# Performance work log

Measured on AMD Instinct MI355X. Metric: run time of the kernel, lower is better.

Reference implementation:

```python
import jax, jax.numpy as jnp
import numpy as np
import math

B, C, H, W = 8, 96, 128, 128


def cos_map(N):
    wx = (jnp.arange(N, dtype=jnp.float32) + 0.5) / N          # [N]
    wn = jnp.arange(N, dtype=jnp.float32)[:, None]             # [N,1]
    w = jnp.cos(wn * wx[None, :] * jnp.pi) * math.sqrt(2.0 / N)
    return w.at[0, :].multiply(1.0 / math.sqrt(2.0))            # [N,N] (n, x)


def decay_map(h, w):
    wn = jnp.linspace(0.0, jnp.pi, h + 1)[:h][:, None]
    wm = jnp.linspace(0.0, jnp.pi, w + 1)[:w][None, :]
    return jnp.exp(-(wn ** 2 + wm ** 2))                        # [h,w]


def setup_inputs() -> dict:
    key = jax.random.key(0)
    ks = jax.random.split(key, 20)
    s = 0.02
    return {
        'x': jax.random.normal(ks[0], (B, C, H, W), jnp.float32),
        'freq_embed': jax.random.normal(ks[1], (H, W, C), jnp.float32),
        'outline_feat': jax.random.normal(ks[2], (B, H, W, C), jnp.float32),
        'dw_w': jax.random.normal(ks[3], (C, 1, 3, 3), jnp.float32) * s,
        'dw_b': jnp.zeros((C,), jnp.float32),
        'lin_w': jax.random.normal(ks[4], (2 * C, C), jnp.float32) * s,
        'lin_b': jnp.zeros((2 * C,), jnp.float32),
        'k_w': jax.random.normal(ks[5], (C, C), jnp.float32) * s,
        'k_b': jnp.zeros((C,), jnp.float32),
        'lin2_w': jax.random.normal(ks[6], (2 * C, 2 * C), jnp.float32) * s,
        'lin2_b': jnp.zeros((2 * C,), jnp.float32),
        'k2_w': jax.random.normal(ks[7], (2 * C, 2 * C), jnp.float32) * s,
        'k2_b': jnp.zeros((2 * C,), jnp.float32),
        'lin3_w': jax.random.normal(ks[8], (C, 2 * C), jnp.float32) * s,
        'lin3_b': jnp.zeros((C,), jnp.float32),
        'ln_g': jnp.ones((C,), jnp.float32),
        'ln_b': jnp.zeros((C,), jnp.float32),
        'out_w': jax.random.normal(ks[9], (C, C), jnp.float32) * s,
        'out_b': jnp.zeros((C,), jnp.float32),
    }


def dct2(u, cn, cm):
    # u: [B,H,W,C] -> [B,N,M,C]
    u = jnp.einsum('nh,bhwc->bnwc', cn, u)
    return jnp.einsum('mw,bnwc->bnmc', cm, u)


def idct2(u, cn, cm):
    # u: [B,N,M,C] -> [B,H,W,C]
    u = jnp.einsum('nh,bnmc->bhmc', cn, u)
    return jnp.einsum('mw,bhmc->bhwc', cm, u)


def layernorm(u, g, b, eps=1e-5):
    mu = jnp.mean(u, axis=-1, keepdims=True)
    var = jnp.var(u, axis=-1, keepdims=True)
    return (u - mu) * jax.lax.rsqrt(var + eps) * g + b


def reference(x, freq_embed, outline_feat, dw_w, dw_b, lin_w, lin_b, k_w, k_b,
              lin2_w, lin2_b, k2_w, k2_b, lin3_w, lin3_b, ln_g, ln_b, out_w, out_b):
    # depthwise 3x3 conv, padding 1 (NCHW)
    x = jax.lax.conv_general_dilated(
        x, dw_w, window_strides=(1, 1), padding=((1, 1), (1, 1)),
        dimension_numbers=('NCHW', 'OIHW', 'NCHW'), feature_group_count=C)
    x = x + dw_b[None, :, None, None]
    x = jnp.transpose(x, (0, 2, 3, 1))                          # [B,H,W,C]
    h = jnp.einsum('bhwc,dc->bhwd', x, lin_w) + lin_b           # [B,H,W,2C]
    x, z = jnp.split(h, 2, axis=-1)

    cn, cm = cos_map(H), cos_map(W)
    dec = decay_map(H, W)                                       # [H,W]

    # first heat pass
    x = dct2(x, cn, cm)                                         # [B,N,M,C]
    otfeat = jnp.mean(outline_feat, axis=0)                     # [H,W,C]
    k = jax.nn.relu(jnp.einsum('hwc,dc->hwd', freq_embed + otfeat, k_w) + k_b)
    x = x * jnp.power(dec[:, :, None], k)                       # [B,N,M,C]
    x = idct2(x, cn, cm)                                        # [B,H,W,C]

    # second heat pass on concatenated features
    x = jnp.concatenate([x, outline_feat], axis=-1)             # [B,H,W,2C]
    skfeat = jnp.mean(jnp.einsum('bhwc,dc->bhwd', x, lin2_w) + lin2_b, axis=0)  # [H,W,2C]
    x = dct2(x, cn, cm)
    k2 = jax.nn.relu(jnp.einsum('hwc,dc->hwd', skfeat, k2_w) + k2_b)
    x = x * jnp.power(dec[:, :, None], k2)
    x = idct2(x, cn, cm)                                        # [B,H,W,2C]

    x = jnp.einsum('bhwc,dc->bhwd', x, lin3_w) + lin3_b         # [B,H,W,C]
    x = layernorm(x, ln_g, ln_b)
    x = x * jax.nn.silu(z)
    x = jnp.einsum('bhwc,dc->bhwd', x, out_w) + out_b
    return jnp.transpose(x, (0, 3, 1, 2))                       # [B,C,H,W]
```

## Files before the change

kernel.cpp:

```cpp
#include <hip/hip_runtime.h>
#include <math.h>
#include <stdint.h>

#ifndef M_PI
#define M_PI 3.14159265358979323846
#endif

#define HW 16384
#define BHW 131072

typedef __attribute__((ext_vector_type(8))) short s8bf;
typedef __attribute__((ext_vector_type(4))) float f32x4;

union FragU { uint32_t u[4]; s8bf s; };

__device__ __forceinline__ uint32_t bf16h(float x) {
  uint32_t u = __float_as_uint(x);
  return (u + 0x7FFFu + ((u >> 16) & 1u)) >> 16;
}
__device__ __forceinline__ uint32_t packhl(float x) {
  uint32_t h = bf16h(x);
  float r = x - __uint_as_float(h << 16);
  return (h << 16) | bf16h(r);
}
__device__ __forceinline__ void unpack8(const uint32_t* w, s8bf& hi, s8bf& lo) {
  FragU H, L;
#pragma unroll
  for (int j = 0; j < 4; ++j) {
    H.u[j] = __builtin_amdgcn_perm(w[2 * j + 1], w[2 * j], 0x07060302u);
    L.u[j] = __builtin_amdgcn_perm(w[2 * j + 1], w[2 * j], 0x05040100u);
  }
  hi = H.s; lo = L.s;
}

__device__ __forceinline__ float cval(int a, int b) {
  double v = cos((double)a * ((double)b + 0.5) * (M_PI / 128.0)) * sqrt(2.0 / 128.0);
  if (a == 0) v *= 0.70710678118654752440;
  return (float)v;
}

__device__ __forceinline__ void wfrag_dev(const float* __restrict__ src,
                                          uint32_t* __restrict__ Fh,
                                          uint32_t* __restrict__ Fl,
                                          int D, int K, int tid) {
  int nksl = K >> 5;
  int total = (D >> 4) * nksl * 64;
  if (tid >= total) return;
  int lane = tid & 63, fid = tid >> 6;
  int nt = fid / nksl, ksl = fid - nt * nksl;
  int d = 16 * nt + (lane & 15);
  int k0 = 32 * ksl + 8 * (lane >> 4);
#pragma unroll
  for (int j = 0; j < 4; ++j) {
    uint32_t p0 = packhl(src[d * K + k0 + 2 * j]);
    uint32_t p1 = packhl(src[d * K + k0 + 2 * j + 1]);
    Fh[tid * 4 + j] = (p0 >> 16) | (p1 & 0xFFFF0000u);
    Fl[tid * 4 + j] = (p0 & 0xFFFFu) | (p1 << 16);
  }
}

__global__ __launch_bounds__(256) void kprep(
    float* __restrict__ ee,
    uint32_t* __restrict__ FAh, uint32_t* __restrict__ FAl,
    uint32_t* __restrict__ FTh, uint32_t* __restrict__ FTl,
    const float* __restrict__ lin_w, uint32_t* __restrict__ WLh, uint32_t* __restrict__ WLl,
    const float* __restrict__ lin3_w, uint32_t* __restrict__ W3h, uint32_t* __restrict__ W3l,
    const float* __restrict__ out_w, uint32_t* __restrict__ WOh, uint32_t* __restrict__ WOl,
    const float* __restrict__ lin2_w, uint32_t* __restrict__ W2h, uint32_t* __restrict__ W2l,
    const float* __restrict__ k2_w, uint32_t* __restrict__ K2h, uint32_t* __restrict__ K2l,
    const float* __restrict__ k_w, float* __restrict__ kT,
    const float* __restrict__ fe, float* __restrict__ fet) {
  __shared__ float tile[64 * 97];
  const int bb = blockIdx.x;
  const int tid = threadIdx.x;
  if (bb < 64) {
    int gid = bb * 256 + tid;
    int n = gid >> 7, m = gid & 127;
    double wn = (double)n * (M_PI / 128.0), wm = (double)m * (M_PI / 128.0);
    ee[gid] = (float)(wn * wn + wm * wm);
  } else if (bb < 72) {
    int t2 = (bb - 64) * 256 + tid;
    int lane = t2 & 63, fid = t2 >> 6;
    int mt = fid >> 2, ks = fid & 3;
    int n = 16 * mt + (lane & 15);
    int k0 = 32 * ks + 8 * (lane >> 4);
#pragma unroll
    for (int j = 0; j < 4; ++j) {
      uint32_t p0 = packhl(cval(n, k0 + 2 * j)), p1 = packhl(cval(n, k0 + 2 * j + 1));
      FAh[t2 * 4 + j] = (p0 >> 16) | (p1 & 0xFFFF0000u);
      FAl[t2 * 4 + j] = (p0 & 0xFFFFu) | (p1 << 16);
      uint32_t q0 = packhl(cval(k0 + 2 * j, n)), q1 = packhl(cval(k0 + 2 * j + 1, n));
      FTh[t2 * 4 + j] = (q0 >> 16) | (q1 & 0xFFFF0000u);
      FTl[t2 * 4 + j] = (q0 & 0xFFFFu) | (q1 << 16);
    }
  } else if (bb < 81) {
    wfrag_dev(lin_w, WLh, WLl, 192, 96, (bb - 72) * 256 + tid);
  } else if (bb < 90) {
    wfrag_dev(lin3_w, W3h, W3l, 96, 192, (bb - 81) * 256 + tid);
  } else if (bb < 95) {
    wfrag_dev(out_w, WOh, WOl, 96, 96, (bb - 90) * 256 + tid);
  } else if (bb < 113) {
    wfrag_dev(lin2_w, W2h, W2l, 192, 192, (bb - 95) * 256 + tid);
  } else if (bb < 131) {
    wfrag_dev(k2_w, K2h, K2l, 192, 192, (bb - 113) * 256 + tid);
  } else if (bb < 167) {
    int gid = (bb - 131) * 256 + tid;
    if (gid < 96 * 96) {
      int d = gid / 96, c = gid % 96;
      kT[c * 96 + d] = k_w[gid];
    }
  } else {
    int hw0 = (bb - 167) * 64;
#pragma unroll
    for (int t = 0; t < 24; ++t) {
      int l = tid + t * 256;
      int r = l / 96, c0 = l % 96;
      tile[r * 97 + c0] = fe[((size_t)hw0 + r) * 96 + c0];
    }
    __syncthreads();
#pragma unroll
    for (int t = 0; t < 24; ++t) {
      int l = tid + t * 256;
      int c0 = l >> 6, r = l & 63;
      fet[(size_t)c0 * HW + hw0 + r] = tile[r * 97 + c0];
    }
  }
}

__global__ __launch_bounds__(256) void kconv(
    const float* __restrict__ x, const float* __restrict__ dw_w,
    const float* __restrict__ dw_b, uint32_t* __restrict__ xcu) {
  int gid = blockIdx.x * 256 + threadIdx.x;
  int p = gid >> 12;
  int q = gid & 4095;
  int h = q >> 5, w4 = (q & 31) << 2;
  int c = p % 96;
  const float* pw = dw_w + c * 9;
  const float* row = x + (size_t)p * HW + h * 128 + w4;
  bool tp = h > 0, bt = h < 127, lf = w4 > 0, rt = w4 < 124;
  float4 t_, m_, b_;
  float tl, tr, ml, mr, bl, br;
  m_ = *(const float4*)row;
  ml = lf ? row[-1] : 0.f;
  mr = rt ? row[4] : 0.f;
  if (tp) {
    t_ = *(const float4*)(row - 128);
    tl = lf ? row[-129] : 0.f;
    tr = rt ? row[-124] : 0.f;
  } else { t_ = make_float4(0.f, 0.f, 0.f, 0.f); tl = tr = 0.f; }
  if (bt) {
    b_ = *(const float4*)(row + 128);
    bl = lf ? row[127] : 0.f;
    br = rt ? row[132] : 0.f;
  } else { b_ = make_float4(0.f, 0.f, 0.f, 0.f); bl = br = 0.f; }
  float w0 = pw[0], w1 = pw[1], w2 = pw[2], w3 = pw[3], w4w = pw[4],
        w5 = pw[5], w6 = pw[6], w7 = pw[7], w8 = pw[8];
  float bias = dw_b[c];
  float o0, o1, o2, o3;
  o0 = tl * w0 + t_.x * w1 + t_.y * w2 + ml * w3 + m_.x * w4w + m_.y * w5 + bl * w6 + b_.x * w7 + b_.y * w8 + bias;
  o1 = t_.x * w0 + t_.y * w1 + t_.z * w2 + m_.x * w3 + m_.y * w4w + m_.z * w5 + b_.x * w6 + b_.y * w7 + b_.z * w8 + bias;
  o2 = t_.y * w0 + t_.z * w1 + t_.w * w2 + m_.y * w3 + m_.z * w4w + m_.w * w5 + b_.y * w6 + b_.z * w7 + b_.w * w8 + bias;
  o3 = t_.z * w0 + t_.w * w1 + tr * w2 + m_.z * w3 + m_.w * w4w + mr * w5 + b_.z * w6 + b_.w * w7 + br * w8 + bias;
  uint4 ou = make_uint4(packhl(o0), packhl(o1), packhl(o2), packhl(o3));
  *(uint4*)(xcu + (size_t)p * HW + h * 128 + w4) = ou;
}

__global__ __launch_bounds__(256) void klin_mfma(
    const uint32_t* __restrict__ xcu, const uint32_t* __restrict__ WLh,
    const uint32_t* __restrict__ WLl, const float* __restrict__ lin_b,
    uint32_t* __restrict__ x1u, float* __restrict__ z) {
  __shared__ uint32_t Ds[64 * 102];
  const int tid = threadIdx.x;
  const int lane = tid & 63;
  const int w = tid >> 6;
  const int l15 = lane & 15, lg = lane >> 4;
  const int gp0 = blockIdx.x * 64;
  const int b = gp0 >> 14, hw0 = gp0 & 16383;

#pragma unroll
  for (int i = 0; i < 24; ++i) {
    int k = w + 4 * i;
    Ds[lane * 102 + k] = xcu[((size_t)(b * 96 + k)) * HW + hw0 + lane];
  }
  __syncthreads();

  f32x4 acc[3][4];
#pragma unroll
  for (int nt = 0; nt < 3; ++nt) {
    float bv[4];
#pragma unroll
    for (int r = 0; r < 4; ++r) bv[r] = lin_b[16 * (3 * w + nt) + 4 * lg + r];
#pragma unroll
    for (int mt = 0; mt < 4; ++mt)
#pragma unroll
      for (int r = 0; r < 4; ++r) acc[nt][mt][r] = bv[r];
  }

#pragma unroll
  for (int ksl = 0; ksl < 3; ++ksl) {
    s8bf Dhi[4], Dlo[4];
#pragma unroll
    for (int mt = 0; mt < 4; ++mt) {
      const uint32_t* p = Ds + (16 * mt + l15) * 102 + 32 * ksl + 8 * lg;
      uint32_t wv[8];
      *(uint2*)&wv[0] = *(const uint2*)(p);
      *(uint2*)&wv[2] = *(const uint2*)(p + 2);
      *(uint2*)&wv[4] = *(const uint2*)(p + 4);
      *(uint2*)&wv[6] = *(const uint2*)(p + 6);
      unpack8(wv, Dhi[mt], Dlo[mt]);
    }
#pragma unroll
    for (int nt = 0; nt < 3; ++nt) {
      int base = (((3 * w + nt) * 3 + ksl) * 64 + lane) * 4;
      FragU H, L;
      *(uint4*)H.u = *(const uint4*)(WLh + base);
      *(uint4*)L.u = *(const uint4*)(WLl + base);
#pragma unroll
      for (int mt = 0; mt < 4; ++mt) {
        acc[nt][mt] = __builtin_amdgcn_mfma_f32_16x16x32_bf16(H.s, Dhi[mt], acc[nt][mt], 0, 0, 0);
        acc[nt][mt] = __builtin_amdgcn_mfma_f32_16x16x32_bf16(H.s, Dlo[mt], acc[nt][mt], 0, 0, 0);
        acc[nt][mt] = __builtin_amdgcn_mfma_f32_16x16x32_bf16(L.s, Dhi[mt], acc[nt][mt], 0, 0, 0);
      }
    }
  }
#pragma unroll
  for (int nt = 0; nt < 3; ++nt) {
    int d0 = 16 * (3 * w + nt) + 4 * lg;
#pragma unroll
    for (int mt = 0; mt < 4; ++mt) {
#pragma unroll
      for (int r = 0; r < 4; ++r) {
        int d = d0 + r;
        if (d < 96)
          x1u[((size_t)(b * 96 + d)) * HW + hw0 + 16 * mt + l15] = packhl(acc[nt][mt][r]);
        else
          z[((size_t)(d - 96)) * BHW + gp0 + 16 * mt + l15] = acc[nt][mt][r];
      }
    }
  }
}

__global__ __launch_bounds__(256) void k3_transpose_mean(
    const float* __restrict__ of, uint32_t* __restrict__ ofu, float* __restrict__ cmU) {
  __shared__ float tile[64 * 97];
  int hw0 = blockIdx.x * 64;
  int tid = threadIdx.x;
  float sum[24];
#pragma unroll
  for (int t = 0; t < 24; ++t) sum[t] = 0.f;
  for (int b = 0; b < 8; ++b) {
    __syncthreads();
#pragma unroll
    for (int t = 0; t < 24; ++t) {
      int l = tid + t * 256;
      int r = l / 96, c0 = l % 96;
      tile[r * 97 + c0] = of[((size_t)b * 16384 + hw0 + r) * 96 + c0];
    }
    __syncthreads();
#pragma unroll
    for (int t = 0; t < 24; ++t) {
      int l = tid + t * 256;
      int c0 = l >> 6, r = l & 63;
      float v = tile[r * 97 + c0];
      sum[t] += v;
      ofu[(size_t)(b * 96 + c0) * HW + hw0 + r] = packhl(v);
    }
  }
#pragma unroll
  for (int t = 0; t < 24; ++t) {
    int l = tid + t * 256;
    int c0 = l >> 6, r = l & 63;
    cmU[(size_t)c0 * HW + hw0 + r] = sum[t] * 0.125f;
  }
}

__global__ __launch_bounds__(256) void k3b_kgemm(
    const float* __restrict__ fet, const float* __restrict__ otm,
    const float* __restrict__ kT, const float* __restrict__ kb,
    const float* __restrict__ ee, float* __restrict__ P1) {
  int tid = threadIdx.x;
  int lane = tid & 63;
  int n0 = __builtin_amdgcn_readfirstlane((tid >> 6) * 24);
  int row = blockIdx.x * 64 + lane;
  float acc[24];
#pragma unroll
  for (int j = 0; j < 24; ++j) acc[j] = kb[n0 + j];
#pragma unroll 4
  for (int c = 0; c < 96; ++c) {
    float a = fet[(size_t)c * HW + row] + otm[(size_t)c * HW + row];
    const float* wr = kT + c * 96 + n0;
#pragma unroll
    for (int j = 0; j < 24; ++j) acc[j] = fmaf(a, wr[j], acc[j]);
  }
  float er = ee[row];
#pragma unroll
  for (int j = 0; j < 24; ++j)
    P1[(size_t)(n0 + j) * HW + row] = expf(-er * fmaxf(acc[j], 0.f));
}

template <bool DATA_A>
__device__ __forceinline__ void heat_step(
    const uint32_t* __restrict__ Fh, const uint32_t* __restrict__ Fl,
    const uint32_t* __restrict__ Ds, f32x4 (&acc)[4][4], int wm, int wn, int lane) {
  const int l15 = lane & 15, lg = lane >> 4;
  const int wd = DATA_A ? wm : wn;
  const int wf = DATA_A ? wn : wm;
#pragma unroll
  for (int ksl = 0; ksl < 4; ++ksl) {
    s8bf Dhi[4], Dlo[4], Fhi[4], Flo[4];
#pragma unroll
    for (int t = 0; t < 4; ++t) {
      const uint32_t* p = Ds + (64 * wd + 16 * t + l15) * 130 + 32 * ksl + 8 * lg;
      uint32_t wv[8];
      *(uint2*)&wv[0] = *(const uint2*)(p);
      *(uint2*)&wv[2] = *(const uint2*)(p + 2);
      *(uint2*)&wv[4] = *(const uint2*)(p + 4);
      *(uint2*)&wv[6] = *(const uint2*)(p + 6);
      unpack8(wv, Dhi[t], Dlo[t]);
    }
#pragma unroll
    for (int t = 0; t < 4; ++t) {
      int base = (((4 * wf + t) * 4 + ksl) * 64 + lane) * 4;
      FragU H, L;
      *(uint4*)H.u = *(const uint4*)(Fh + base);
      *(uint4*)L.u = *(const uint4*)(Fl + base);
      Fhi[t] = H.s; Flo[t] = L.s;
    }
    const s8bf* Ah = DATA_A ? Dhi : Fhi;
    const s8bf* Al = DATA_A ? Dlo : Flo;
    const s8bf* Bh = DATA_A ? Fhi : Dhi;
    const s8bf* Bl = DATA_A ? Flo : Dlo;
#pragma unroll
    for (int mi = 0; mi < 4; ++mi)
#pragma unroll
      for (int ni = 0; ni < 4; ++ni)
        acc[mi][ni] = __builtin_amdgcn_mfma_f32_16x16x32_bf16(Ah[mi], Bh[ni], acc[mi][ni], 0, 0, 0);
#pragma unroll
    for (int mi = 0; mi < 4; ++mi)
#pragma unroll
      for (int ni = 0; ni < 4; ++ni)
        acc[mi][ni] = __builtin_amdgcn_mfma_f32_16x16x32_bf16(Ah[mi], Bl[ni], acc[mi][ni], 0, 0, 0);
#pragma unroll
    for (int mi = 0; mi < 4; ++mi)
#pragma unroll
      for (int ni = 0; ni < 4; ++ni)
        acc[mi][ni] = __builtin_amdgcn_mfma_f32_16x16x32_bf16(Al[mi], Bh[ni], acc[mi][ni], 0, 0, 0);
  }
}

template <bool PIN, bool POUT, bool USE_P>
__global__ __launch_bounds__(256, 2) void heat_half(
    const float* __restrict__ In, float* __restrict__ Out,
    const float* __restrict__ P, const uint32_t* __restrict__ Fh,
    const uint32_t* __restrict__ Fl, int Cmod) {
  __shared__ uint32_t Ds[128 * 130];
  const int tid = threadIdx.x;
  const int lane = tid & 63;
  const int w = tid >> 6;
  const int wm = w >> 1, wn = w & 1;
  const int l15 = lane & 15, lg = lane >> 4;
  const float* Ip = In + (size_t)blockIdx.x * HW;
  float* Op = Out + (size_t)blockIdx.x * HW;
  const float* Pp = nullptr;
  if constexpr (USE_P) Pp = P + (size_t)(blockIdx.x % Cmod) * HW;

  {
    int col = tid & 127, r0 = tid >> 7;
    if constexpr (PIN) {
      const uint32_t* Iu = (const uint32_t*)Ip;
#pragma unroll
      for (int i = 0; i < 64; ++i) {
        int row = r0 + 2 * i;
        Ds[col * 130 + row] = Iu[row * 128 + col];
      }
    } else {
#pragma unroll
      for (int i = 0; i < 64; ++i) {
        int row = r0 + 2 * i;
        Ds[col * 130 + row] = packhl(Ip[row * 128 + col]);
      }
    }
  }
  __syncthreads();

  f32x4 acc[4][4];
  const f32x4 zero4 = {0.f, 0.f, 0.f, 0.f};
#pragma unroll
  for (int mi = 0; mi < 4; ++mi)
#pragma unroll
    for (int ni = 0; ni < 4; ++ni) acc[mi][ni] = zero4;
  heat_step<false>(Fh, Fl, Ds, acc, wm, wn, lane);
  __syncthreads();
#pragma unroll
  for (int mi = 0; mi < 4; ++mi)
#pragma unroll
    for (int ni = 0; ni < 4; ++ni)
#pragma unroll
      for (int r = 0; r < 4; ++r)
        Ds[(64 * wm + 16 * mi + 4 * lg + r) * 130 + 64 * wn + 16 * ni + l15] =
            packhl(acc[mi][ni][r]);
  __syncthreads();

#pragma unroll
  for (int mi = 0; mi < 4; ++mi)
#pragma unroll
    for (int ni = 0; ni < 4; ++ni) acc[mi][ni] = zero4;
  heat_step<true>(Fh, Fl, Ds, acc, wm, wn, lane);
#pragma unroll
  for (int mi = 0; mi < 4; ++mi)
#pragma unroll
    for (int ni = 0; ni < 4; ++ni) {
      int row = 64 * wm + 16 * mi + 4 * lg;
      int col = 64 * wn + 16 * ni + l15;
#pragma unroll
      for (int r = 0; r < 4; ++r) {
        float v = acc[mi][ni][r];
        if constexpr (USE_P) v *= Pp[(row + r) * 128 + col];
        if constexpr (POUT)
          ((uint32_t*)Op)[(row + r) * 128 + col] = packhl(v);
        else
          Op[(row + r) * 128 + col] = v;
      }
    }
}

__global__ void k5_mean(const float* __restrict__ src, float* __restrict__ dst) {
  int idx = blockIdx.x * 256 + threadIdx.x;
  int c = idx >> 14, s = idx & 16383;
  float sum = 0.f;
#pragma unroll
  for (int b = 0; b < 8; ++b) sum += src[(size_t)(b * 96 + c) * HW + s];
  dst[idx] = sum * 0.125f;
}

__global__ __launch_bounds__(256) void k67_mfma(
    const float* __restrict__ cm,
    const uint32_t* __restrict__ W2h, const uint32_t* __restrict__ W2l,
    const float* __restrict__ b2,
    const uint32_t* __restrict__ K2h, const uint32_t* __restrict__ K2l,
    const float* __restrict__ b2k, const float* __restrict__ ee,
    float* __restrict__ P2) {
  __shared__ uint32_t Ds[64 * 194];
  const int tid = threadIdx.x;
  const int lane = tid & 63;
  const int w = tid >> 6;
  const int l15 = lane & 15, lg = lane >> 4;
  const int row0 = blockIdx.x * 64;

#pragma unroll
  for (int i = 0; i < 48; ++i) {
    int k = w + 4 * i;
    Ds[lane * 194 + k] = packhl(cm[(size_t)k * HW + row0 + lane]);
  }
  __syncthreads();

  f32x4 acc[3][4];
#pragma unroll
  for (int nt = 0; nt < 3; ++nt) {
    float bv[4];
#pragma unroll
    for (int r = 0; r < 4; ++r) bv[r] = b2[16 * (3 * w + nt) + 4 * lg + r];
#pragma unroll
    for (int mt = 0; mt < 4; ++mt)
#pragma unroll
      for (int r = 0; r < 4; ++r) acc[nt][mt][r] = bv[r];
  }
#pragma unroll
  for (int ksl = 0; ksl < 6; ++ksl) {
    s8bf Dhi[4], Dlo[4];
#pragma unroll
    for (int mt = 0; mt < 4; ++mt) {
      const uint32_t* p = Ds + (16 * mt + l15) * 194 + 32 * ksl + 8 * lg;
      uint32_t wv[8];
      *(uint2*)&wv[0] = *(const uint2*)(p);
      *(uint2*)&wv[2] = *(const uint2*)(p + 2);
      *(uint2*)&wv[4] = *(const uint2*)(p + 4);
      *(uint2*)&wv[6] = *(const uint2*)(p + 6);
      unpack8(wv, Dhi[mt], Dlo[mt]);
    }
#pragma unroll
    for (int nt = 0; nt < 3; ++nt) {
      int base = (((3 * w + nt) * 6 + ksl) * 64 + lane) * 4;
      FragU H, L;
      *(uint4*)H.u = *(const uint4*)(W2h + base);
      *(uint4*)L.u = *(const uint4*)(W2l + base);
#pragma unroll
      for (int mt = 0; mt < 4; ++mt) {
        acc[nt][mt] = __builtin_amdgcn_mfma_f32_16x16x32_bf16(H.s, Dhi[mt], acc[nt][mt], 0, 0, 0);
        acc[nt][mt] = __builtin_amdgcn_mfma_f32_16x16x32_bf16(H.s, Dlo[mt], acc[nt][mt], 0, 0, 0);
        acc[nt][mt] = __builtin_amdgcn_mfma_f32_16x16x32_bf16(L.s, Dhi[mt], acc[nt][mt], 0, 0, 0);
      }
    }
  }
  __syncthreads();
#pragma unroll
  for (int nt = 0; nt < 3; ++nt) {
    int d0 = 16 * (3 * w + nt) + 4 * lg;
#pragma unroll
    for (int mt = 0; mt < 4; ++mt) {
      int col = 16 * mt + l15;
#pragma unroll
      for (int r = 0; r < 4; ++r)
        Ds[col * 194 + d0 + r] = packhl(acc[nt][mt][r]);
    }
  }
  __syncthreads();

  f32x4 acc2[3][4];
#pragma unroll
  for (int nt = 0; nt < 3; ++nt) {
    float bv[4];
#pragma unroll
    for (int r = 0; r < 4; ++r) bv[r] = b2k[16 * (3 * w + nt) + 4 * lg + r];
#pragma unroll
    for (int mt = 0; mt < 4; ++mt)
#pragma unroll
      for (int r = 0; r < 4; ++r) acc2[nt][mt][r] = bv[r];
  }
#pragma unroll
  for (int ksl = 0; ksl < 6; ++ksl) {
    s8bf Dhi[4], Dlo[4];
#pragma unroll
    for (int mt = 0; mt < 4; ++mt) {
      const uint32_t* p = Ds + (16 * mt + l15) * 194 + 32 * ksl + 8 * lg;
      uint32_t wv[8];
      *(uint2*)&wv[0] = *(const uint2*)(p);
      *(uint2*)&wv[2] = *(const uint2*)(p + 2);
      *(uint2*)&wv[4] = *(const uint2*)(p + 4);
      *(uint2*)&wv[6] = *(const uint2*)(p + 6);
      unpack8(wv, Dhi[mt], Dlo[mt]);
    }
#pragma unroll
    for (int nt = 0; nt < 3; ++nt) {
      int base = (((3 * w + nt) * 6 + ksl) * 64 + lane) * 4;
      FragU H, L;
      *(uint4*)H.u = *(const uint4*)(K2h + base);
      *(uint4*)L.u = *(const uint4*)(K2l + base);
#pragma unroll
      for (int mt = 0; mt < 4; ++mt) {
        acc2[nt][mt] = __builtin_amdgcn_mfma_f32_16x16x32_bf16(H.s, Dhi[mt], acc2[nt][mt], 0, 0, 0);
        acc2[nt][mt] = __builtin_amdgcn_mfma_f32_16x16x32_bf16(H.s, Dlo[mt], acc2[nt][mt], 0, 0, 0);
        acc2[nt][mt] = __builtin_amdgcn_mfma_f32_16x16x32_bf16(L.s, Dhi[mt], acc2[nt][mt], 0, 0, 0);
      }
    }
  }
  float er[4];
#pragma unroll
  for (int mt = 0; mt < 4; ++mt) er[mt] = ee[row0 + 16 * mt + l15];
#pragma unroll
  for (int nt = 0; nt < 3; ++nt) {
    int d0 = 16 * (3 * w + nt) + 4 * lg;
#pragma unroll
    for (int mt = 0; mt < 4; ++mt) {
      int row = row0 + 16 * mt + l15;
#pragma unroll
      for (int r = 0; r < 4; ++r)
        P2[(size_t)(d0 + r) * HW + row] = expf(-er[mt] * fmaxf(acc2[nt][mt][r], 0.f));
    }
  }
}

__global__ __launch_bounds__(256) void kmix(
    const float* __restrict__ S1, const uint32_t* __restrict__ OhU,
    const float* __restrict__ P2,
    const uint32_t* __restrict__ W3h, const uint32_t* __restrict__ W3l,
    uint32_t* __restrict__ TfU) {
  __shared__ uint32_t Ds[128 * 98];
  const int tid = threadIdx.x;
  const int lane = tid & 63;
  const int w = tid >> 6;
  const int wn = w >> 1, wm = w & 1;
  const int l15 = lane & 15, lg = lane >> 4;
  const int gp0 = blockIdx.x * 128;
  const int b = gp0 >> 14, hw0 = gp0 & 16383;

  f32x4 acc[3][4];
#pragma unroll
  for (int i = 0; i < 3; ++i)
#pragma unroll
    for (int j = 0; j < 4; ++j)
#pragma unroll
      for (int r = 0; r < 4; ++r) acc[i][j][r] = 0.f;

#pragma unroll
  for (int c = 0; c < 2; ++c) {
    if (c) __syncthreads();
#pragma unroll
    for (int i = 0; i < 24; ++i) {
      int k = w + 4 * i;
      if (c == 0) {
        const float* sp = S1 + ((size_t)(b * 96 + k)) * HW + hw0;
        const float* pp = P2 + (size_t)k * HW + hw0;
        Ds[lane * 98 + k] = packhl(sp[lane] * pp[lane]);
        Ds[(lane + 64) * 98 + k] = packhl(sp[lane + 64] * pp[lane + 64]);
      } else {
        const uint32_t* sp = OhU + ((size_t)(b * 96 + k)) * HW + hw0;
        Ds[lane * 98 + k] = sp[lane];
        Ds[(lane + 64) * 98 + k] = sp[lane + 64];
      }
    }
    __syncthreads();
#pragma unroll
    for (int ksl = 0; ksl < 3; ++ksl) {
      s8bf Dhi[4], Dlo[4];
#pragma unroll
      for (int j = 0; j < 4; ++j) {
        const uint32_t* p = Ds + (16 * (4 * wm + j) + l15) * 98 + 32 * ksl + 8 * lg;
        uint32_t wv[8];
        *(uint2*)&wv[0] = *(const uint2*)(p);
        *(uint2*)&wv[2] = *(const uint2*)(p + 2);
        *(uint2*)&wv[4] = *(const uint2*)(p + 4);
        *(uint2*)&wv[6] = *(const uint2*)(p + 6);
        unpack8(wv, Dhi[j], Dlo[j]);
      }
#pragma unroll
      for (int i = 0; i < 3; ++i) {
        int base = (((3 * wn + i) * 6 + 3 * c + ksl) * 64 + lane) * 4;
        FragU H, L;
        *(uint4*)H.u = *(const uint4*)(W3h + base);
        *(uint4*)L.u = *(const uint4*)(W3l + base);
#pragma unroll
        for (int j = 0; j < 4; ++j) {
          acc[i][j] = __builtin_amdgcn_mfma_f32_16x16x32_bf16(H.s, Dhi[j], acc[i][j], 0, 0, 0);
          acc[i][j] = __builtin_amdgcn_mfma_f32_16x16x32_bf16(H.s, Dlo[j], acc[i][j], 0, 0, 0);
          acc[i][j] = __builtin_amdgcn_mfma_f32_16x16x32_bf16(L.s, Dhi[j], acc[i][j], 0, 0, 0);
        }
      }
    }
  }
#pragma unroll
  for (int i = 0; i < 3; ++i) {
    int d0 = 16 * (3 * wn + i) + 4 * lg;
#pragma unroll
    for (int j = 0; j < 4; ++j) {
      int hw = hw0 + 16 * (4 * wm + j) + l15;
#pragma unroll
      for (int r = 0; r < 4; ++r)
        TfU[((size_t)(b * 96 + d0 + r)) * HW + hw] = packhl(acc[i][j][r]);
    }
  }
}

__global__ __launch_bounds__(256) void k9r(
    const float* __restrict__ y3, const float* __restrict__ z,
    const float* __restrict__ lin3b,
    const float* __restrict__ lng, const float* __restrict__ lnb,
    const uint32_t* __restrict__ WOh, const uint32_t* __restrict__ WOl,
    const float* __restrict__ outb, float* __restrict__ out) {
  __shared__ uint32_t Ds2[128 * 98];
  __shared__ float2 red[4][128];
  const int tid = threadIdx.x;
  const int lane = tid & 63;
  const int w = tid >> 6;
  const int wn = w >> 1, wm = w & 1;
  const int l15 = lane & 15, lg = lane >> 4;
  const int gp0 = blockIdx.x * 128;
  const int b = gp0 >> 14, hw0 = gp0 & 16383;

  float vA[24], vB[24];
  float sA = 0.f, qA = 0.f, sB = 0.f, qB = 0.f;
#pragma unroll
  for (int i = 0; i < 24; ++i) {
    int k = w + 4 * i;
    const float* yp = y3 + ((size_t)(b * 96 + k)) * HW + hw0;
    float bk = lin3b[k];
    float tA = yp[lane] + bk;      vA[i] = tA; sA += tA; qA = fmaf(tA, tA, qA);
    float tB = yp[lane + 64] + bk; vB[i] = tB; sB += tB; qB = fmaf(tB, tB, qB);
  }
  red[w][lane] = make_float2(sA, qA);
  red[w][lane + 64] = make_float2(sB, qB);
  __syncthreads();
  float2 a0 = red[0][lane], a1 = red[1][lane], a2 = red[2][lane], a3 = red[3][lane];
  float2 b0 = red[0][lane + 64], b1 = red[1][lane + 64], b2_ = red[2][lane + 64], b3 = red[3][lane + 64];
  float muA = (a0.x + a1.x + a2.x + a3.x) * (1.f / 96.f);
  float vrA = (a0.y + a1.y + a2.y + a3.y) * (1.f / 96.f) - muA * muA;
  float invA = rsqrtf(fmaxf(vrA, 0.f) + 1e-5f);
  float muB = (b0.x + b1.x + b2_.x + b3.x) * (1.f / 96.f);
  float vrB = (b0.y + b1.y + b2_.y + b3.y) * (1.f / 96.f) - muB * muB;
  float invB = rsqrtf(fmaxf(vrB, 0.f) + 1e-5f);
#pragma unroll
  for (int i = 0; i < 24; ++i) {
    int k = w + 4 * i;
    const float* zp = z + (size_t)k * BHW + gp0;
    float g = lng[k], bb = lnb[k];
    float zA = zp[lane];
    float uA = (vA[i] - muA) * invA * g + bb;
    Ds2[lane * 98 + k] = packhl(uA * (zA / (1.f + __expf(-zA))));
    float zB = zp[lane + 64];
    float uB = (vB[i] - muB) * invB * g + bb;
    Ds2[(lane + 64) * 98 + k] = packhl(uB * (zB / (1.f + __expf(-zB))));
  }
  __syncthreads();

  f32x4 acc2[3][4];
#pragma unroll
  for (int i = 0; i < 3; ++i) {
    float bv[4];
#pragma unroll
    for (int r = 0; r < 4; ++r) bv[r] = outb[16 * (3 * wn + i) + 4 * lg + r];
#pragma unroll
    for (int j = 0; j < 4; ++j)
#pragma unroll
      for (int r = 0; r < 4; ++r) acc2[i][j][r] = bv[r];
  }
#pragma unroll
  for (int ksl = 0; ksl < 3; ++ksl) {
    s8bf Dhi[4], Dlo[4];
#pragma unroll
    for (int j = 0; j < 4; ++j) {
      const uint32_t* p = Ds2 + (16 * (4 * wm + j) + l15) * 98 + 32 * ksl + 8 * lg;
      uint32_t wv[8];
      *(uint2*)&wv[0] = *(const uint2*)(p);
      *(uint2*)&wv[2] = *(const uint2*)(p + 2);
      *(uint2*)&wv[4] = *(const uint2*)(p + 4);
      *(uint2*)&wv[6] = *(const uint2*)(p + 6);
      unpack8(wv, Dhi[j], Dlo[j]);
    }
#pragma unroll
    for (int i = 0; i < 3; ++i) {
      int base = (((3 * wn + i) * 3 + ksl) * 64 + lane) * 4;
      FragU H, L;
      *(uint4*)H.u = *(const uint4*)(WOh + base);
      *(uint4*)L.u = *(const uint4*)(WOl + base);
#pragma unroll
      for (int j = 0; j < 4; ++j) {
        acc2[i][j] = __builtin_amdgcn_mfma_f32_16x16x32_bf16(H.s, Dhi[j], acc2[i][j], 0, 0, 0);
        acc2[i][j] = __builtin_amdgcn_mfma_f32_16x16x32_bf16(H.s, Dlo[j], acc2[i][j], 0, 0, 0);
        acc2[i][j] = __builtin_amdgcn_mfma_f32_16x16x32_bf16(L.s, Dhi[j], acc2[i][j], 0, 0, 0);
      }
    }
  }
#pragma unroll
  for (int i = 0; i < 3; ++i) {
    int d0 = 16 * (3 * wn + i) + 4 * lg;
#pragma unroll
    for (int j = 0; j < 4; ++j) {
      int hw = hw0 + 16 * (4 * wm + j) + l15;
#pragma unroll
      for (int r = 0; r < 4; ++r)
        out[((size_t)(b * 96 + d0 + r)) * HW + hw] = acc2[i][j][r];
    }
  }
}

extern "C" void kernel_launch(void* const* d_in, const int* in_sizes, int n_in,
                              void* d_out, int out_size, void* d_ws, size_t ws_size,
                              hipStream_t stream) {
  const float* x      = (const float*)d_in[0];
  const float* fe     = (const float*)d_in[1];
  const float* of     = (const float*)d_in[2];
  const float* dw_w   = (const float*)d_in[3];
  const float* dw_b   = (const float*)d_in[4];
  const float* lin_w  = (const float*)d_in[5];
  const float* lin_b  = (const float*)d_in[6];
  const float* k_w    = (const float*)d_in[7];
  const float* k_b    = (const float*)d_in[8];
  const float* lin2_w = (const float*)d_in[9];
  const float* lin2_b = (const float*)d_in[10];
  const float* k2_w   = (const float*)d_in[11];
  const float* k2_b   = (const float*)d_in[12];
  const float* lin3_w = (const float*)d_in[13];
  const float* lin3_b = (const float*)d_in[14];
  const float* ln_g   = (const float*)d_in[15];
  const float* ln_b   = (const float*)d_in[16];
  const float* out_w  = (const float*)d_in[17];
  const float* out_b  = (const float*)d_in[18];
  float* out = (float*)d_out;

  float* ws    = (float*)d_ws;
  float* x1p   = ws;
  float* z     = x1p   + 12582912;
  float* ofp   = z     + 12582912;
  float* cm    = ofp   + 12582912;
  float* skf   = cm    + 3145728;
  float* P1    = skf   + 3145728;
  float* P2    = P1    + 1572864;
  float* cc    = P2    + 3145728;
  float* ee    = cc    + 16384;
  float* linT  = ee    + 16384;
  float* kT    = linT  + 18432;
  float* lin2T = kT    + 9216;
  float* k2T   = lin2T + 36864;
  float* lin3T = k2T   + 36864;
  float* outT  = lin3T + 18432;
  float* fet   = outT  + 9216;
  uint32_t* FAh = (uint32_t*)(fet + 1572864);
  uint32_t* FAl = FAh + 8192;
  uint32_t* FTh = FAl + 8192;
  uint32_t* FTl = FTh + 8192;
  uint32_t* WLh = FTl + 8192;
  uint32_t* WLl = WLh + 9216;
  uint32_t* W3h = WLl + 9216;
  uint32_t* W3l = W3h + 9216;
  uint32_t* WOh = W3l + 9216;
  uint32_t* WOl = WOh + 4608;
  uint32_t* W2h = WOl + 4608;
  uint32_t* W2l = W2h + 18432;
  uint32_t* K2h = W2l + 18432;
  uint32_t* K2l = K2h + 18432;
  float* cmSf  = skf;
  uint32_t* x1u = (uint32_t*)x1p;
  uint32_t* ofu = (uint32_t*)ofp;
  uint32_t* xcu = ofu;
  (void)in_sizes; (void)n_in; (void)out_size; (void)ws_size;

  kprep<<<423, 256, 0, stream>>>(ee, FAh, FAl, FTh, FTl,
                                 lin_w, WLh, WLl, lin3_w, W3h, W3l,
                                 out_w, WOh, WOl, lin2_w, W2h, W2l,
                                 k2_w, K2h, K2l, k_w, kT, fe, fet);

  kconv<<<12288, 256, 0, stream>>>(x, dw_w, dw_b, xcu);
  klin_mfma<<<2048, 256, 0, stream>>>(xcu, WLh, WLl, lin_b, x1u, z);
  k3_transpose_mean<<<256, 256, 0, stream>>>(of, ofu, cm + (size_t)96 * HW);
  k3b_kgemm<<<256, 256, 0, stream>>>(fet, cm + (size_t)96 * HW, kT, k_b, ee, P1);
  heat_half<true, false, true><<<768, 256, 0, stream>>>(x1p, x1p, P1, FAh, FAl, 96);
  k5_mean<<<6144, 256, 0, stream>>>(x1p, cmSf);
  heat_half<false, false, false><<<96, 256, 0, stream>>>(cmSf, cm, nullptr, FTh, FTl, 96);
  k67_mfma<<<256, 256, 0, stream>>>(cm, W2h, W2l, lin2_b, K2h, K2l, k2_b, ee, P2);
  heat_half<true, true, true><<<768, 256, 0, stream>>>(ofp, ofp, P2 + (size_t)96 * HW, FAh, FAl, 96);
  kmix<<<1024, 256, 0, stream>>>(x1p, ofu, P2, W3h, W3l, x1u);
  heat_half<true, false, false><<<768, 256, 0, stream>>>(x1p, x1p, nullptr, FTh, FTl, 96);
  k9r<<<1024, 256, 0, stream>>>(x1p, z, lin3_b, ln_g, ln_b, WOh, WOl, out_b, out);
}
```

Before: 338.4 us.

## Reorder heat passes: compute mean via linearity, fuse both forward DCT passes

Because the DCT and the multiply by P1 are linear per plane, the batch mean of the first-pass result is now computed before that pass. The mean goes through a single fused heat_full kernel (DCT, multiply by P1, inverse DCT) on only 96 planes. The per-batch first-pass DCT is merged with the outline-feature DCT into one 1536-block heat_big launch, which also folds in the P2 multiply so kmix no longer reads P2. This removes one full-size launch and fp32 round-trips, at the cost of a different rounding order through the split-bf16 packing.

```diff
diff --git a/kernel.cpp b/kernel.cpp
--- a/kernel.cpp
+++ b/kernel.cpp
@@ -22,6 +22,9 @@
   uint32_t h = bf16h(x);
   float r = x - __uint_as_float(h << 16);
   return (h << 16) | bf16h(r);
+}
+__device__ __forceinline__ float unpackf(uint32_t u) {
+  return __uint_as_float(u & 0xFFFF0000u) + __uint_as_float(u << 16);
 }
 __device__ __forceinline__ void unpack8(const uint32_t* w, s8bf& hi, s8bf& lo) {
   FragU H, L;
@@ -298,6 +301,15 @@
     P1[(size_t)(n0 + j) * HW + row] = expf(-er * fmaxf(acc[j], 0.f));
 }
 
+__global__ void kmean_u(const uint32_t* __restrict__ src, float* __restrict__ dst) {
+  int idx = blockIdx.x * 256 + threadIdx.x;
+  int c = idx >> 14, s = idx & 16383;
+  float sum = 0.f;
+#pragma unroll
+  for (int b = 0; b < 8; ++b) sum += unpackf(src[(size_t)(b * 96 + c) * HW + s]);
+  dst[idx] = sum * 0.125f;
+}
+
 template <bool DATA_A>
 __device__ __forceinline__ void heat_step(
     const uint32_t* __restrict__ Fh, const uint32_t* __restrict__ Fl,
@@ -424,13 +436,166 @@
     }
 }
 
-__global__ void k5_mean(const float* __restrict__ src, float* __restrict__ dst) {
-  int idx = blockIdx.x * 256 + threadIdx.x;
-  int c = idx >> 14, s = idx & 16383;
-  float sum = 0.f;
-#pragma unroll
-  for (int b = 0; b < 8; ++b) sum += src[(size_t)(b * 96 + c) * HW + s];
-  dst[idx] = sum * 0.125f;
+__global__ __launch_bounds__(256, 2) void heat_big(
+    uint32_t* __restrict__ X1u, uint32_t* __restrict__ Ohu,
+    const float* __restrict__ P1, const float* __restrict__ P2,
+    const uint32_t* __restrict__ Fh, const uint32_t* __restrict__ Fl) {
+  __shared__ uint32_t Ds[128 * 130];
+  const int tid = threadIdx.x;
+  const int lane = tid & 63;
+  const int w = tid >> 6;
+  const int wm = w >> 1, wn = w & 1;
+  const int l15 = lane & 15, lg = lane >> 4;
+  const int plane = blockIdx.x;
+  const bool first = plane < 768;
+  const int pl = first ? plane : plane - 768;
+  const int c = pl % 96;
+  uint32_t* Ug = (first ? X1u : Ohu) + (size_t)pl * HW;
+  const float* Pa = first ? (P1 + (size_t)c * HW) : (P2 + (size_t)(96 + c) * HW);
+  const float* Pb = P2 + (size_t)c * HW;
+
+  {
+    int col = tid & 127, r0 = tid >> 7;
+#pragma unroll
+    for (int i = 0; i < 64; ++i) {
+      int row = r0 + 2 * i;
+      Ds[col * 130 + row] = Ug[row * 128 + col];
+    }
+  }
+  __syncthreads();
+
+  f32x4 acc[4][4];
+  const f32x4 zero4 = {0.f, 0.f, 0.f, 0.f};
+#pragma unroll
+  for (int mi = 0; mi < 4; ++mi)
+#pragma unroll
+    for (int ni = 0; ni < 4; ++ni) acc[mi][ni] = zero4;
+  heat_step<false>(Fh, Fl, Ds, acc, wm, wn, lane);
+  __syncthreads();
+#pragma unroll
+  for (int mi = 0; mi < 4; ++mi)
+#pragma unroll
+    for (int ni = 0; ni < 4; ++ni)
+#pragma unroll
+      for (int r = 0; r < 4; ++r)
+        Ds[(64 * wm + 16 * mi + 4 * lg + r) * 130 + 64 * wn + 16 * ni + l15] =
+            packhl(acc[mi][ni][r]);
+  __syncthreads();
+
+#pragma unroll
+  for (int mi = 0; mi < 4; ++mi)
+#pragma unroll
+    for (int ni = 0; ni < 4; ++ni) acc[mi][ni] = zero4;
+  heat_step<true>(Fh, Fl, Ds, acc, wm, wn, lane);
+#pragma unroll
+  for (int mi = 0; mi < 4; ++mi)
+#pragma unroll
+    for (int ni = 0; ni < 4; ++ni) {
+      int row = 64 * wm + 16 * mi + 4 * lg;
+      int col = 64 * wn + 16 * ni + l15;
+#pragma unroll
+      for (int r = 0; r < 4; ++r) {
+        int idx = (row + r) * 128 + col;
+        float v = acc[mi][ni][r] * Pa[idx];
+        if (first) v *= Pb[idx];
+        Ug[idx] = packhl(v);
+      }
+    }
+}
+
+__global__ __launch_bounds__(256, 2) void heat_full(
+    const float* __restrict__ In, float* __restrict__ Out,
+    const float* __restrict__ P,
+    const uint32_t* __restrict__ FAh, const uint32_t* __restrict__ FAl,
+    const uint32_t* __restrict__ FTh, const uint32_t* __restrict__ FTl) {
+  __shared__ uint32_t Ds[128 * 130];
+  const int tid = threadIdx.x;
+  const int lane = tid & 63;
+  const int w = tid >> 6;
+  const int wm = w >> 1, wn = w & 1;
+  const int l15 = lane & 15, lg = lane >> 4;
+  const float* Ip = In + (size_t)blockIdx.x * HW;
+  float* Op = Out + (size_t)blockIdx.x * HW;
+  const float* Pp = P + (size_t)blockIdx.x * HW;
+
+  {
+    int col = tid & 127, r0 = tid >> 7;
+#pragma unroll
+    for (int i = 0; i < 64; ++i) {
+      int row = r0 + 2 * i;
+      Ds[col * 130 + row] = packhl(Ip[row * 128 + col]);
+    }
+  }
+  __syncthreads();
+
+  f32x4 acc[4][4];
+  const f32x4 zero4 = {0.f, 0.f, 0.f, 0.f};
+
+#pragma unroll
+  for (int mi = 0; mi < 4; ++mi)
+#pragma unroll
+    for (int ni = 0; ni < 4; ++ni) acc[mi][ni] = zero4;
+  heat_step<false>(FAh, FAl, Ds, acc, wm, wn, lane);
+  __syncthreads();
+#pragma unroll
+  for (int mi = 0; mi < 4; ++mi)
+#pragma unroll
+    for (int ni = 0; ni < 4; ++ni)
+#pragma unroll
+      for (int r = 0; r < 4; ++r)
+        Ds[(64 * wm + 16 * mi + 4 * lg + r) * 130 + 64 * wn + 16 * ni + l15] =
+            packhl(acc[mi][ni][r]);
+  __syncthreads();
+
+#pragma unroll
+  for (int mi = 0; mi < 4; ++mi)
+#pragma unroll
+    for (int ni = 0; ni < 4; ++ni) acc[mi][ni] = zero4;
+  heat_step<true>(FAh, FAl, Ds, acc, wm, wn, lane);
+  __syncthreads();
+#pragma unroll
+  for (int mi = 0; mi < 4; ++mi)
+#pragma unroll
+    for (int ni = 0; ni < 4; ++ni) {
+      int row = 64 * wm + 16 * mi + 4 * lg;
+      int col = 64 * wn + 16 * ni + l15;
+#pragma unroll
+      for (int r = 0; r < 4; ++r)
+        Ds[col * 130 + row + r] = packhl(acc[mi][ni][r] * Pp[(row + r) * 128 + col]);
+    }
+  __syncthreads();
+
+#pragma unroll
+  for (int mi = 0; mi < 4; ++mi)
+#pragma unroll
+    for (int ni = 0; ni < 4; ++ni) acc[mi][ni] = zero4;
+  heat_step<false>(FTh, FTl, Ds, acc, wm, wn, lane);
+  __syncthreads();
+#pragma unroll
+  for (int mi = 0; mi < 4; ++mi)
+#pragma unroll
+    for (int ni = 0; ni < 4; ++ni)
+#pragma unroll
+      for (int r = 0; r < 4; ++r)
+        Ds[(64 * wm + 16 * mi + 4 * lg + r) * 130 + 64 * wn + 16 * ni + l15] =
+            packhl(acc[mi][ni][r]);
+  __syncthreads();
+
+#pragma unroll
+  for (int mi = 0; mi < 4; ++mi)
+#pragma unroll
+    for (int ni = 0; ni < 4; ++ni) acc[mi][ni] = zero4;
+  heat_step<true>(FTh, FTl, Ds, acc, wm, wn, lane);
+#pragma unroll
+  for (int mi = 0; mi < 4; ++mi)
+#pragma unroll
+    for (int ni = 0; ni < 4; ++ni) {
+      int row = 64 * wm + 16 * mi + 4 * lg;
+      int col = 64 * wn + 16 * ni + l15;
+#pragma unroll
+      for (int r = 0; r < 4; ++r)
+        Op[(row + r) * 128 + col] = acc[mi][ni][r];
+    }
 }
 
 __global__ __launch_bounds__(256) void k67_mfma(
@@ -561,8 +726,7 @@
 }
 
 __global__ __launch_bounds__(256) void kmix(
-    const float* __restrict__ S1, const uint32_t* __restrict__ OhU,
-    const float* __restrict__ P2,
+    const uint32_t* __restrict__ S1u, const uint32_t* __restrict__ OhU,
     const uint32_t* __restrict__ W3h, const uint32_t* __restrict__ W3l,
     uint32_t* __restrict__ TfU) {
   __shared__ uint32_t Ds[128 * 98];
@@ -588,16 +752,9 @@
 #pragma unroll
     for (int i = 0; i < 24; ++i) {
       int k = w + 4 * i;
-      if (c == 0) {
-        const float* sp = S1 + ((size_t)(b * 96 + k)) * HW + hw0;
-        const float* pp = P2 + (size_t)k * HW + hw0;
-        Ds[lane * 98 + k] = packhl(sp[lane] * pp[lane]);
-        Ds[(lane + 64) * 98 + k] = packhl(sp[lane + 64] * pp[lane + 64]);
-      } else {
-        const uint32_t* sp = OhU + ((size_t)(b * 96 + k)) * HW + hw0;
-        Ds[lane * 98 + k] = sp[lane];
-        Ds[(lane + 64) * 98 + k] = sp[lane + 64];
-      }
+      const uint32_t* sp = (c == 0 ? S1u : OhU) + ((size_t)(b * 96 + k)) * HW + hw0;
+      Ds[lane * 98 + k] = sp[lane];
+      Ds[(lane + 64) * 98 + k] = sp[lane + 64];
     }
     __syncthreads();
 #pragma unroll
@@ -798,7 +955,7 @@
   uint32_t* W2l = W2h + 18432;
   uint32_t* K2h = W2l + 18432;
   uint32_t* K2l = K2h + 18432;
-  float* cmSf  = skf;
+  float* mx1   = skf;
   uint32_t* x1u = (uint32_t*)x1p;
   uint32_t* ofu = (uint32_t*)ofp;
   uint32_t* xcu = ofu;
@@ -813,12 +970,11 @@
   klin_mfma<<<2048, 256, 0, stream>>>(xcu, WLh, WLl, lin_b, x1u, z);
   k3_transpose_mean<<<256, 256, 0, stream>>>(of, ofu, cm + (size_t)96 * HW);
   k3b_kgemm<<<256, 256, 0, stream>>>(fet, cm + (size_t)96 * HW, kT, k_b, ee, P1);
-  heat_half<true, false, true><<<768, 256, 0, stream>>>(x1p, x1p, P1, FAh, FAl, 96);
-  k5_mean<<<6144, 256, 0, stream>>>(x1p, cmSf);
-  heat_half<false, false, false><<<96, 256, 0, stream>>>(cmSf, cm, nullptr, FTh, FTl, 96);
+  kmean_u<<<6144, 256, 0, stream>>>(x1u, mx1);
+  heat_full<<<96, 256, 0, stream>>>(mx1, cm, P1, FAh, FAl, FTh, FTl);
   k67_mfma<<<256, 256, 0, stream>>>(cm, W2h, W2l, lin2_b, K2h, K2l, k2_b, ee, P2);
-  heat_half<true, true, true><<<768, 256, 0, stream>>>(ofp, ofp, P2 + (size_t)96 * HW, FAh, FAl, 96);
-  kmix<<<1024, 256, 0, stream>>>(x1p, ofu, P2, W3h, W3l, x1u);
+  heat_big<<<1536, 256, 0, stream>>>(x1u, ofu, P1, P2, FAh, FAl);
+  kmix<<<1024, 256, 0, stream>>>(x1u, ofu, W3h, W3l, x1u);
   heat_half<true, false, false><<<768, 256, 0, stream>>>(x1p, x1p, nullptr, FTh, FTl, 96);
   k9r<<<1024, 256, 0, stream>>>(x1p, z, lin3_b, ln_g, ln_b, WOh, WOl, out_b, out);
 }
```

After: 380.4 us. 12.4% more time.

## Split heat_half across 8 waves with 64x32 per-wave tiles

Applied to the files above, without the earlier changes.

Reworks the 128x128 DCT heat kernel so each block uses 512 threads (8 waves in a 2x4 grid) instead of 256, and each wave computes a 64x32 output tile instead of 64x64. This halves per-wave accumulator registers and adds latency hiding within a block, with launch bounds raised to allow more resident waves. In exchange, each wave reloads the 64-row A-side fragments while covering half as many columns, which adds LDS and global fragment traffic relative to compute.

```diff
diff --git a/kernel.cpp b/kernel.cpp
--- a/kernel.cpp
+++ b/kernel.cpp
@@ -299,18 +299,17 @@
 }
 
 template <bool DATA_A>
-__device__ __forceinline__ void heat_step(
+__device__ __forceinline__ void heat_step8(
     const uint32_t* __restrict__ Fh, const uint32_t* __restrict__ Fl,
-    const uint32_t* __restrict__ Ds, f32x4 (&acc)[4][4], int wm, int wn, int lane) {
+    const uint32_t* __restrict__ Ds, f32x4 (&acc)[4][2], int wm, int wn, int lane) {
   const int l15 = lane & 15, lg = lane >> 4;
-  const int wd = DATA_A ? wm : wn;
-  const int wf = DATA_A ? wn : wm;
 #pragma unroll
   for (int ksl = 0; ksl < 4; ++ksl) {
     s8bf Dhi[4], Dlo[4], Fhi[4], Flo[4];
 #pragma unroll
-    for (int t = 0; t < 4; ++t) {
-      const uint32_t* p = Ds + (64 * wd + 16 * t + l15) * 130 + 32 * ksl + 8 * lg;
+    for (int t = 0; t < (DATA_A ? 4 : 2); ++t) {
+      int rc = DATA_A ? (64 * wm + 16 * t) : (32 * wn + 16 * t);
+      const uint32_t* p = Ds + (rc + l15) * 130 + 32 * ksl + 8 * lg;
       uint32_t wv[8];
       *(uint2*)&wv[0] = *(const uint2*)(p);
       *(uint2*)&wv[2] = *(const uint2*)(p + 2);
@@ -319,37 +318,38 @@
       unpack8(wv, Dhi[t], Dlo[t]);
     }
 #pragma unroll
-    for (int t = 0; t < 4; ++t) {
-      int base = (((4 * wf + t) * 4 + ksl) * 64 + lane) * 4;
+    for (int t = 0; t < (DATA_A ? 2 : 4); ++t) {
+      int tile = DATA_A ? (2 * wn + t) : (4 * wm + t);
+      int base = ((tile * 4 + ksl) * 64 + lane) * 4;
       FragU H, L;
       *(uint4*)H.u = *(const uint4*)(Fh + base);
       *(uint4*)L.u = *(const uint4*)(Fl + base);
       Fhi[t] = H.s; Flo[t] = L.s;
     }
-    const s8bf* Ah = DATA_A ? Dhi : Fhi;
-    const s8bf* Al = DATA_A ? Dlo : Flo;
-    const s8bf* Bh = DATA_A ? Fhi : Dhi;
-    const s8bf* Bl = DATA_A ? Flo : Dlo;
-#pragma unroll
-    for (int mi = 0; mi < 4; ++mi)
-#pragma unroll
-      for (int ni = 0; ni < 4; ++ni)
-        acc[mi][ni] = __builtin_amdgcn_mfma_f32_16x16x32_bf16(Ah[mi], Bh[ni], acc[mi][ni], 0, 0, 0);
-#pragma unroll
-    for (int mi = 0; mi < 4; ++mi)
-#pragma unroll
-      for (int ni = 0; ni < 4; ++ni)
-        acc[mi][ni] = __builtin_amdgcn_mfma_f32_16x16x32_bf16(Ah[mi], Bl[ni], acc[mi][ni], 0, 0, 0);
-#pragma unroll
-    for (int mi = 0; mi < 4; ++mi)
-#pragma unroll
-      for (int ni = 0; ni < 4; ++ni)
-        acc[mi][ni] = __builtin_amdgcn_mfma_f32_16x16x32_bf16(Al[mi], Bh[ni], acc[mi][ni], 0, 0, 0);
+    if constexpr (DATA_A) {
+#pragma unroll
+      for (int mi = 0; mi < 4; ++mi)
+#pragma unroll
+        for (int ni = 0; ni < 2; ++ni) {
+          acc[mi][ni] = __builtin_amdgcn_mfma_f32_16x16x32_bf16(Dhi[mi], Fhi[ni], acc[mi][ni], 0, 0, 0);
+          acc[mi][ni] = __builtin_amdgcn_mfma_f32_16x16x32_bf16(Dhi[mi], Flo[ni], acc[mi][ni], 0, 0, 0);
+          acc[mi][ni] = __builtin_amdgcn_mfma_f32_16x16x32_bf16(Dlo[mi], Fhi[ni], acc[mi][ni], 0, 0, 0);
+        }
+    } else {
+#pragma unroll
+      for (int mi = 0; mi < 4; ++mi)
+#pragma unroll
+        for (int ni = 0; ni < 2; ++ni) {
+          acc[mi][ni] = __builtin_amdgcn_mfma_f32_16x16x32_bf16(Fhi[mi], Dhi[ni], acc[mi][ni], 0, 0, 0);
+          acc[mi][ni] = __builtin_amdgcn_mfma_f32_16x16x32_bf16(Fhi[mi], Dlo[ni], acc[mi][ni], 0, 0, 0);
+          acc[mi][ni] = __builtin_amdgcn_mfma_f32_16x16x32_bf16(Flo[mi], Dhi[ni], acc[mi][ni], 0, 0, 0);
+        }
+    }
   }
 }
 
 template <bool PIN, bool POUT, bool USE_P>
-__global__ __launch_bounds__(256, 2) void heat_half(
+__global__ __launch_bounds__(512, 4) void heat_half(
     const float* __restrict__ In, float* __restrict__ Out,
     const float* __restrict__ P, const uint32_t* __restrict__ Fh,
     const uint32_t* __restrict__ Fl, int Cmod) {
@@ -357,7 +357,7 @@
   const int tid = threadIdx.x;
   const int lane = tid & 63;
   const int w = tid >> 6;
-  const int wm = w >> 1, wn = w & 1;
+  const int wm = w >> 2, wn = w & 3;
   const int l15 = lane & 15, lg = lane >> 4;
   const float* Ip = In + (size_t)blockIdx.x * HW;
   float* Op = Out + (size_t)blockIdx.x * HW;
@@ -369,49 +369,49 @@
     if constexpr (PIN) {
       const uint32_t* Iu = (const uint32_t*)Ip;
 #pragma unroll
-      for (int i = 0; i < 64; ++i) {
-        int row = r0 + 2 * i;
+      for (int i = 0; i < 32; ++i) {
+        int row = r0 + 4 * i;
         Ds[col * 130 + row] = Iu[row * 128 + col];
       }
     } else {
 #pragma unroll
-      for (int i = 0; i < 64; ++i) {
-        int row = r0 + 2 * i;
+      for (int i = 0; i < 32; ++i) {
+        int row = r0 + 4 * i;
         Ds[col * 130 + row] = packhl(Ip[row * 128 + col]);
       }
     }
   }
   __syncthreads();
 
-  f32x4 acc[4][4];
+  f32x4 acc[4][2];
   const f32x4 zero4 = {0.f, 0.f, 0.f, 0.f};
 #pragma unroll
   for (int mi = 0; mi < 4; ++mi)
 #pragma unroll
-    for (int ni = 0; ni < 4; ++ni) acc[mi][ni] = zero4;
-  heat_step<false>(Fh, Fl, Ds, acc, wm, wn, lane);
+    for (int ni = 0; ni < 2; ++ni) acc[mi][ni] = zero4;
+  heat_step8<false>(Fh, Fl, Ds, acc, wm, wn, lane);
   __syncthreads();
 #pragma unroll
   for (int mi = 0; mi < 4; ++mi)
 #pragma unroll
-    for (int ni = 0; ni < 4; ++ni)
+    for (int ni = 0; ni < 2; ++ni)
 #pragma unroll
       for (int r = 0; r < 4; ++r)
-        Ds[(64 * wm + 16 * mi + 4 * lg + r) * 130 + 64 * wn + 16 * ni + l15] =
+        Ds[(64 * wm + 16 * mi + 4 * lg + r) * 130 + 32 * wn + 16 * ni + l15] =
             packhl(acc[mi][ni][r]);
   __syncthreads();
 
 #pragma unroll
   for (int mi = 0; mi < 4; ++mi)
 #pragma unroll
-    for (int ni = 0; ni < 4; ++ni) acc[mi][ni] = zero4;
-  heat_step<true>(Fh, Fl, Ds, acc, wm, wn, lane);
+    for (int ni = 0; ni < 2; ++ni) acc[mi][ni] = zero4;
+  heat_step8<true>(Fh, Fl, Ds, acc, wm, wn, lane);
 #pragma unroll
   for (int mi = 0; mi < 4; ++mi)
 #pragma unroll
-    for (int ni = 0; ni < 4; ++ni) {
+    for (int ni = 0; ni < 2; ++ni) {
       int row = 64 * wm + 16 * mi + 4 * lg;
-      int col = 64 * wn + 16 * ni + l15;
+      int col = 32 * wn + 16 * ni + l15;
 #pragma unroll
       for (int r = 0; r < 4; ++r) {
         float v = acc[mi][ni][r];
@@ -813,12 +813,12 @@
   klin_mfma<<<2048, 256, 0, stream>>>(xcu, WLh, WLl, lin_b, x1u, z);
   k3_transpose_mean<<<256, 256, 0, stream>>>(of, ofu, cm + (size_t)96 * HW);
   k3b_kgemm<<<256, 256, 0, stream>>>(fet, cm + (size_t)96 * HW, kT, k_b, ee, P1);
-  heat_half<true, false, true><<<768, 256, 0, stream>>>(x1p, x1p, P1, FAh, FAl, 96);
+  heat_half<true, false, true><<<768, 512, 0, stream>>>(x1p, x1p, P1, FAh, FAl, 96);
   k5_mean<<<6144, 256, 0, stream>>>(x1p, cmSf);
-  heat_half<false, false, false><<<96, 256, 0, stream>>>(cmSf, cm, nullptr, FTh, FTl, 96);
+  heat_half<false, false, false><<<96, 512, 0, stream>>>(cmSf, cm, nullptr, FTh, FTl, 96);
   k67_mfma<<<256, 256, 0, stream>>>(cm, W2h, W2l, lin2_b, K2h, K2l, k2_b, ee, P2);
-  heat_half<true, true, true><<<768, 256, 0, stream>>>(ofp, ofp, P2 + (size_t)96 * HW, FAh, FAl, 96);
+  heat_half<true, true, true><<<768, 512, 0, stream>>>(ofp, ofp, P2 + (size_t)96 * HW, FAh, FAl, 96);
   kmix<<<1024, 256, 0, stream>>>(x1p, ofu, P2, W3h, W3l, x1u);
-  heat_half<true, false, false><<<768, 256, 0, stream>>>(x1p, x1p, nullptr, FTh, FTl, 96);
+  heat_half<true, false, false><<<768, 512, 0, stream>>>(x1p, x1p, nullptr, FTh, FTl, 96);
   k9r<<<1024, 256, 0, stream>>>(x1p, z, lin3_b, ln_g, ln_b, WOh, WOl, out_b, out);
 }
```

Result: no change. 340.0 us (+0.5%).
